# Kernel tuning notes

Measured on AMD Instinct MI355X. Metric: run time of the kernel, lower is better.

The kernel has to match this reference:

```python
import jax, jax.numpy as jnp
import numpy as np
import math

B, L, D, H, DFF, GEOM = 4, 768, 512, 8, 2048, 7
DK = D // H


def layer_norm(x, scale, bias, eps=1e-5):
    mu = jnp.mean(x, axis=-1, keepdims=True)
    var = jnp.mean(jnp.square(x - mu), axis=-1, keepdims=True)
    return (x - mu) * jax.lax.rsqrt(var + eps) * scale + bias


def setup_inputs() -> dict:
    key = jax.random.key(0)
    ks = jax.random.split(key, 20)
    s = 0.02
    inp = {
        "x": jax.random.normal(ks[0], (B, L, D), jnp.float32),
        "geom_feat": jax.random.uniform(ks[1], (B, L, L, GEOM), jnp.float32),
        "mask": jnp.ones((B, L), jnp.int32),
        # weights stored (in, out): y = x @ W + b, math-equivalent to torch Linear
        "Wq": jax.random.normal(ks[2], (D, D), jnp.float32) * s,
        "bq": jnp.zeros((D,), jnp.float32),
        "Wk": jax.random.normal(ks[3], (D, D), jnp.float32) * s,
        "bk": jnp.zeros((D,), jnp.float32),
        "Wv": jax.random.normal(ks[4], (D, D), jnp.float32) * s,
        "bv": jnp.zeros((D,), jnp.float32),
        "Wo": jax.random.normal(ks[5], (D, D), jnp.float32) * s,
        "bo": jnp.zeros((D,), jnp.float32),
        "Wg": jax.random.normal(ks[6], (GEOM, H), jnp.float32) * s,
        "bg": jnp.zeros((H,), jnp.float32),
        "Wgcn": jax.random.normal(ks[7], (D, D), jnp.float32) * s,
        "bgcn": jnp.zeros((D,), jnp.float32),
        "gcn_gate": jnp.float32(0.5),
        "W1": jax.random.normal(ks[8], (D, 2 * DFF), jnp.float32) * s,
        "b1": jnp.zeros((2 * DFF,), jnp.float32),
        "W2": jax.random.normal(ks[9], (DFF, D), jnp.float32) * s,
        "b2": jnp.zeros((D,), jnp.float32),
        "ln1_s": jnp.ones((D,), jnp.float32),
        "ln1_b": jnp.zeros((D,), jnp.float32),
        "ln2_s": jnp.ones((D,), jnp.float32),
        "ln2_b": jnp.zeros((D,), jnp.float32),
    }
    return inp


def reference(x, geom_feat, mask,
              Wq, bq, Wk, bk, Wv, bv, Wo, bo, Wg, bg,
              Wgcn, bgcn, gcn_gate, W1, b1, W2, b2,
              ln1_s, ln1_b, ln2_s, ln2_b):
    m = mask.astype(x.dtype)  # (B, L)
    # normalized adjacency from distance channel
    adj = jnp.exp(-geom_feat[..., 0] / 5.0)                 # (B, L, L)
    adj = adj * (m[:, :, None] * m[:, None, :])
    adj = adj / (jnp.sum(adj, axis=-1, keepdims=True) + 1e-6)

    h = layer_norm(x, ln1_s, ln1_b)                          # (B, L, D)

    # structure-guided attention
    Q = (h @ Wq + bq).reshape(B, L, H, DK)
    K = (h @ Wk + bk).reshape(B, L, H, DK)
    V = (h @ Wv + bv).reshape(B, L, H, DK)
    scores = jnp.einsum('blhd,bmhd->bhlm', Q, K) / math.sqrt(DK)
    bias = jnp.einsum('blmg,gh->bhlm', geom_feat, Wg) + bg[None, :, None, None]
    scores = scores + bias
    scores = jnp.where(mask[:, None, None, :] == 0, -10000.0, scores)
    attn = jax.nn.softmax(scores, axis=-1)
    ctx = jnp.einsum('bhlm,bmhd->blhd', attn, V).reshape(B, L, D)
    attn_out = ctx @ Wo + bo

    # dense GCN branch (exact GELU, matching torch nn.GELU default)
    g = h @ Wgcn + bgcn
    gcn_out = jax.nn.gelu(jnp.einsum('blm,bmd->bld', adj, g), approximate=False)

    x = x + attn_out + gcn_out * gcn_gate

    # gated feed-forward
    h2 = layer_norm(x, ln2_s, ln2_b)
    ff = h2 @ W1 + b1
    u, gate = ff[..., :DFF], ff[..., DFF:]
    x = x + (u * jax.nn.sigmoid(gate)) @ W2 + b2
    return x
```

## Files before the change

kernel.cpp:

```cpp
#include <hip/hip_runtime.h>
#include <hip/hip_bf16.h>
#include <math.h>

typedef __attribute__((ext_vector_type(8))) short bf8;
typedef __attribute__((ext_vector_type(4))) float f4;

typedef const __attribute__((address_space(1))) void* gas_t;
typedef __attribute__((address_space(3))) void* las_t;

__device__ __forceinline__ ushort f2bf(float x){
  union { float f; unsigned u; } v; v.f = x;
  unsigned r = (v.u + 0x7fffu + ((v.u >> 16) & 1u)) >> 16;
  return (ushort)r;
}
__device__ __forceinline__ float bf2f(ushort b){
  union { unsigned u; float f; } v; v.u = ((unsigned)b) << 16;
  return v.f;
}

struct GP {
  const ushort* A; long lda; long aBatch;
  const ushort* Bt; long ldb; long bBatch;
  const ushort* Bt2;
  int K;
  float* outf; ushort* outb;
  ushort* o1; ushort* o2; ushort* o3;
  const float* bias0; const float* bias1; const float* bias2; const float* bias3;
  const float* addf;
};

enum { EP_QKVG=0, EP_GCN, EP_ATTNOUT, EP_FF, EP_FINAL };

template<int EPI, bool DUAL>
__global__ __launch_bounds__(256)
void gemm_k(GP p) {
  __shared__ __align__(16) ushort As[64*64];
  __shared__ __align__(16) ushort Bs[64*64];
  __shared__ __align__(16) ushort Bs2[DUAL ? 64*64 : 8];
  const int tid = threadIdx.x;
  const int lane = tid & 63, w = tid >> 6;
  const int wm = w >> 1, wn = w & 1;
  const int g = lane >> 4, lr = lane & 15;
  const int lr8 = lane >> 3, sc = lane & 7;
  const int bm = blockIdx.x, bn = blockIdx.y, z = blockIdx.z;

  const ushort* Ab  = p.A  + (long)z*p.aBatch + (long)bm*64*p.lda;
  const ushort* Btb = p.Bt + (long)z*p.bBatch + (long)bn*64*p.ldb;
  const ushort* Bt2b = DUAL ? (p.Bt2 + (long)bn*64*p.ldb) : (const ushort*)nullptr;

  f4 acc[2][2] = {};
  f4 acc2[DUAL?2:1][DUAL?2:1] = {};

  for (int k0 = 0; k0 < p.K; k0 += 64) {
    #pragma unroll
    for (int i = 0; i < 2; ++i) {
      int row = i*32 + w*8 + lr8;
      const ushort* gsA = Ab + (long)row*p.lda + k0 + ((sc ^ (row & 7)) << 3);
      __builtin_amdgcn_global_load_lds((gas_t)gsA, (las_t)&As[(i*32 + w*8)*64], 16, 0, 0);
      const ushort* gsB = Btb + (long)row*p.ldb + k0 + ((sc ^ (row & 7)) << 3);
      __builtin_amdgcn_global_load_lds((gas_t)gsB, (las_t)&Bs[(i*32 + w*8)*64], 16, 0, 0);
      if (DUAL) {
        const ushort* gsB2 = Bt2b + (long)row*p.ldb + k0 + ((sc ^ (row & 7)) << 3);
        __builtin_amdgcn_global_load_lds((gas_t)gsB2, (las_t)&Bs2[(i*32 + w*8)*64], 16, 0, 0);
      }
    }
    __syncthreads();

    #pragma unroll
    for (int kw = 0; kw < 2; ++kw) {
      const int chunk = kw*4 + g;
      bf8 af[2], bfr[2], bf2[2];
      #pragma unroll
      for (int f = 0; f < 2; ++f) {
        int ar = wm*32 + f*16 + lr;
        af[f]  = *(const bf8*)&As[ar*64 + ((chunk ^ (ar & 7)) << 3)];
        int br = wn*32 + f*16 + lr;
        bfr[f] = *(const bf8*)&Bs[br*64 + ((chunk ^ (br & 7)) << 3)];
        if (DUAL) bf2[f] = *(const bf8*)&Bs2[br*64 + ((chunk ^ (br & 7)) << 3)];
      }
      #pragma unroll
      for (int fm = 0; fm < 2; ++fm)
        #pragma unroll
        for (int fn = 0; fn < 2; ++fn) {
          acc[fm][fn] = __builtin_amdgcn_mfma_f32_16x16x32_bf16(af[fm], bfr[fn], acc[fm][fn], 0,0,0);
          if (DUAL) acc2[fm][fn] = __builtin_amdgcn_mfma_f32_16x16x32_bf16(af[fm], bf2[fn], acc2[fm][fn], 0,0,0);
        }
    }
    __syncthreads();
  }

  #pragma unroll
  for (int fm = 0; fm < 2; ++fm)
  #pragma unroll
  for (int fn = 0; fn < 2; ++fn)
  #pragma unroll
  for (int i = 0; i < 4; ++i) {
    int grow = bm*64 + wm*32 + fm*16 + g*4 + i;
    int gcol = bn*64 + wn*32 + fn*16 + lr;
    float v = acc[fm][fn][i];
    if constexpr (EPI == EP_QKVG) {
      int sec = gcol >> 9, cc = gcol & 511;
      const float* bp = sec==0 ? p.bias0 : sec==1 ? p.bias1 : sec==2 ? p.bias2 : p.bias3;
      v += bp[cc];
      ushort bvv = f2bf(v);
      if (sec == 0)      p.outb[(long)grow*512 + cc] = bvv;
      else if (sec == 1) p.o1[(long)grow*512 + cc] = bvv;
      else {
        int b = grow / 768, l = grow - b*768;
        ushort* dst = (sec==2) ? p.o2 : p.o3;
        dst[((long)b*512 + cc)*768 + l] = bvv;
      }
    } else if constexpr (EPI == EP_GCN) {
      float ge = 0.5f * v * (1.f + erff(v * 0.70710678118f));
      p.outf[((long)z*768 + grow)*512 + gcol] = ge;
    } else if constexpr (EPI == EP_ATTNOUT) {
      p.outf[(long)grow*512 + gcol] = v + p.bias0[gcol];
    } else if constexpr (EPI == EP_FF) {
      float u = v + p.bias0[gcol];
      float gt = acc2[fm][fn][i] + p.bias0[2048 + gcol];
      float a = u / (1.f + expf(-gt));
      p.outb[(long)grow*2048 + gcol] = f2bf(a);
    } else if constexpr (EPI == EP_FINAL) {
      long idx = (long)grow*512 + gcol;
      p.outf[idx] = p.addf[idx] + v + p.bias0[gcol];
    }
  }
}

__global__ __launch_bounds__(256) void flash_k(const ushort* __restrict__ qg,
    const ushort* __restrict__ kg, const ushort* __restrict__ vtg,
    const ushort* __restrict__ biasg, ushort* __restrict__ ctx) {
  __shared__ __align__(16) ushort Ks[64*64];
  __shared__ __align__(16) ushort Vs[64*64];
  __shared__ __align__(16) ushort Ps[64*64];
  const int tid = threadIdx.x;
  const int lane = tid & 63, w = tid >> 6;
  const int g = lane >> 4, lr = lane & 15;
  const int qt = blockIdx.x, bh = blockIdx.y;
  const int b = bh >> 3, h = bh & 7;
  const int q0 = qt*64;

  bf8 aq[2];
  #pragma unroll
  for (int kk = 0; kk < 2; ++kk)
    aq[kk] = *(const bf8*)&qg[(long)(b*768 + q0 + w*16 + lr)*512 + h*64 + kk*32 + g*8];

  f4 o[4] = {};
  float mrow[4], lsum[4];
  #pragma unroll
  for (int i = 0; i < 4; ++i) { mrow[i] = -1e30f; lsum[i] = 0.f; }

  const int srow = tid >> 3, sc = tid & 7;

  for (int kt = 0; kt < 12; ++kt) {
    const int kbase = kt*64;
    #pragma unroll
    for (int ps = 0; ps < 2; ++ps) {
      int r = srow + ps*32;
      int sw = ((sc ^ (r & 7)) * 8);
      *(uint4*)&Ks[r*64 + sw] = *(const uint4*)&kg[(long)(b*768 + kbase + r)*512 + h*64 + sc*8];
      *(uint4*)&Vs[r*64 + sw] = *(const uint4*)&vtg[((long)b*512 + h*64 + r)*768 + kbase + sc*8];
    }
    __syncthreads();

    f4 s[4] = {};
    #pragma unroll
    for (int kn = 0; kn < 4; ++kn) {
      #pragma unroll
      for (int kk = 0; kk < 2; ++kk) {
        int row = kn*16 + lr;
        bf8 bk = *(const bf8*)&Ks[row*64 + (((kk*4+g) ^ (row & 7)) * 8)];
        s[kn] = __builtin_amdgcn_mfma_f32_16x16x32_bf16(aq[kk], bk, s[kn], 0,0,0);
      }
    }

    float pv[4][4];
    #pragma unroll
    for (int kn = 0; kn < 4; ++kn)
      #pragma unroll
      for (int i = 0; i < 4; ++i) {
        float bv = bf2f(biasg[((long)bh*768 + q0 + w*16 + g*4 + i)*768 + kbase + kn*16 + lr]);
        pv[kn][i] = s[kn][i]*0.125f + bv;
      }

    #pragma unroll
    for (int i = 0; i < 4; ++i) {
      float m2 = fmaxf(fmaxf(pv[0][i], pv[1][i]), fmaxf(pv[2][i], pv[3][i]));
      #pragma unroll
      for (int off = 1; off < 16; off <<= 1) m2 = fmaxf(m2, __shfl_xor(m2, off, 64));
      float mnew = fmaxf(mrow[i], m2);
      float scale = __expf(mrow[i] - mnew);
      mrow[i] = mnew;
      float psum = 0.f;
      #pragma unroll
      for (int kn = 0; kn < 4; ++kn) { pv[kn][i] = __expf(pv[kn][i] - mnew); psum += pv[kn][i]; }
      #pragma unroll
      for (int off = 1; off < 16; off <<= 1) psum += __shfl_xor(psum, off, 64);
      lsum[i] = lsum[i]*scale + psum;
      #pragma unroll
      for (int dn = 0; dn < 4; ++dn) o[dn][i] *= scale;
    }

    #pragma unroll
    for (int kn = 0; kn < 4; ++kn)
      #pragma unroll
      for (int i = 0; i < 4; ++i) {
        int row = w*16 + g*4 + i;
        int col = kn*16 + lr;
        Ps[row*64 + (((col >> 3) ^ (row & 7)) * 8) + (col & 7)] = f2bf(pv[kn][i]);
      }

    #pragma unroll
    for (int kk2 = 0; kk2 < 2; ++kk2) {
      int prow = w*16 + lr;
      bf8 pa = *(const bf8*)&Ps[prow*64 + (((kk2*4+g) ^ (prow & 7)) * 8)];
      #pragma unroll
      for (int dn = 0; dn < 4; ++dn) {
        int vrow = dn*16 + lr;
        bf8 bv = *(const bf8*)&Vs[vrow*64 + (((kk2*4+g) ^ (vrow & 7)) * 8)];
        o[dn] = __builtin_amdgcn_mfma_f32_16x16x32_bf16(pa, bv, o[dn], 0,0,0);
      }
    }
    __syncthreads();
  }

  #pragma unroll
  for (int i = 0; i < 4; ++i) {
    float inv = 1.f / lsum[i];
    #pragma unroll
    for (int dn = 0; dn < 4; ++dn)
      ctx[(long)(b*768 + q0 + w*16 + g*4 + i)*512 + h*64 + dn*16 + lr] = f2bf(o[dn][i]*inv);
  }
}

__global__ __launch_bounds__(256) void transpose_bf(const float* src, ushort* dst, int R, int C) {
  __shared__ float t[32][33];
  int r0 = blockIdx.x*32, c0 = blockIdx.y*32;
  int tr = threadIdx.x >> 5, tc = threadIdx.x & 31;
  #pragma unroll
  for (int i = 0; i < 4; ++i)
    t[tr + i*8][tc] = src[(long)(r0 + tr + i*8)*C + c0 + tc];
  __syncthreads();
  #pragma unroll
  for (int i = 0; i < 4; ++i)
    dst[(long)(c0 + tr + i*8)*R + r0 + tc] = f2bf(t[tc][tr + i*8]);
}

__global__ __launch_bounds__(256) void ln_k(const float* x, const float* gam, const float* bet, ushort* out) {
  int row = blockIdx.x, tid = threadIdx.x;
  long base = (long)row*512;
  float v0 = x[base+tid], v1 = x[base+tid+256];
  float s = v0+v1, q = v0*v0 + v1*v1;
  #pragma unroll
  for (int off=32; off>=1; off>>=1){ s += __shfl_down(s,off,64); q += __shfl_down(q,off,64); }
  __shared__ float red[8];
  int lane=tid&63, wave=tid>>6;
  if (lane==0){ red[wave]=s; red[4+wave]=q; }
  __syncthreads();
  if (tid==0){ red[0]=red[0]+red[1]+red[2]+red[3]; red[4]=red[4]+red[5]+red[6]+red[7]; }
  __syncthreads();
  float mu = red[0]*(1.f/512.f);
  float var = red[4]*(1.f/512.f) - mu*mu;
  float rs = rsqrtf(var + 1e-5f);
  out[base+tid]     = f2bf((v0-mu)*rs*gam[tid]     + bet[tid]);
  out[base+tid+256] = f2bf((v1-mu)*rs*gam[tid+256] + bet[tid+256]);
}

__global__ __launch_bounds__(256) void resid_ln2_k(const float* x, const float* ao, const float* gc,
    const float* gatep, const float* gam, const float* bet, float* xmid, ushort* h2) {
  int row = blockIdx.x, tid = threadIdx.x;
  long base = (long)row*512;
  float gate = *gatep;
  float v0 = x[base+tid]     + ao[base+tid]     + gc[base+tid]*gate;
  float v1 = x[base+tid+256] + ao[base+tid+256] + gc[base+tid+256]*gate;
  xmid[base+tid] = v0; xmid[base+tid+256] = v1;
  float s = v0+v1, q = v0*v0 + v1*v1;
  #pragma unroll
  for (int off=32; off>=1; off>>=1){ s += __shfl_down(s,off,64); q += __shfl_down(q,off,64); }
  __shared__ float red[8];
  int lane=tid&63, wave=tid>>6;
  if (lane==0){ red[wave]=s; red[4+wave]=q; }
  __syncthreads();
  if (tid==0){ red[0]=red[0]+red[1]+red[2]+red[3]; red[4]=red[4]+red[5]+red[6]+red[7]; }
  __syncthreads();
  float mu = red[0]*(1.f/512.f);
  float var = red[4]*(1.f/512.f) - mu*mu;
  float rs = rsqrtf(var + 1e-5f);
  h2[base+tid]     = f2bf((v0-mu)*rs*gam[tid]     + bet[tid]);
  h2[base+tid+256] = f2bf((v1-mu)*rs*gam[tid+256] + bet[tid+256]);
}

__global__ __launch_bounds__(256) void adjbias_k(const float* __restrict__ geom,
    const int* __restrict__ mask, const float* __restrict__ Wg, const float* __restrict__ bg,
    ushort* __restrict__ adjb, ushort* __restrict__ biasb) {
  int bl = blockIdx.x;
  int b = bl / 768, l = bl - b*768;
  int tid = threadIdx.x;
  __shared__ float wgs[56];
  __shared__ float bgs[8];
  if (tid < 56) wgs[tid] = Wg[tid];
  if (tid < 8)  bgs[tid] = bg[tid];
  __syncthreads();
  float ml = (float)mask[bl];
  float e[3]; float ssum = 0.f;
  #pragma unroll
  for (int j = 0; j < 3; ++j) {
    int m = tid + j*256;
    const float* gp = &geom[((long)bl*768 + m)*7];
    float g0 = gp[0], g1 = gp[1], g2 = gp[2], g3 = gp[3], g4 = gp[4], g5 = gp[5], g6 = gp[6];
    float mm = (float)mask[b*768 + m];
    e[j] = __expf(-g0*0.2f) * mm;
    ssum += e[j];
    #pragma unroll
    for (int hh = 0; hh < 8; ++hh) {
      float bv = bgs[hh] + g0*wgs[hh] + g1*wgs[8+hh] + g2*wgs[16+hh] + g3*wgs[24+hh]
               + g4*wgs[32+hh] + g5*wgs[40+hh] + g6*wgs[48+hh];
      biasb[((long)(b*8+hh)*768 + l)*768 + m] = f2bf(mm != 0.f ? bv : -10000.f);
    }
  }
  #pragma unroll
  for (int off=32; off>=1; off>>=1) ssum += __shfl_down(ssum, off, 64);
  __shared__ float red[4];
  int lane = tid & 63, wave = tid >> 6;
  if (lane == 0) red[wave] = ssum;
  __syncthreads();
  if (tid == 0) red[0] = red[0]+red[1]+red[2]+red[3];
  __syncthreads();
  float inv = ml / (ml*red[0] + 1e-6f);
  #pragma unroll
  for (int j = 0; j < 3; ++j)
    adjb[(long)bl*768 + tid + j*256] = f2bf(e[j] * inv);
}

extern "C" void kernel_launch(void* const* d_in, const int* in_sizes, int n_in,
                              void* d_out, int out_size, void* d_ws, size_t ws_size,
                              hipStream_t stream) {
  const float* x    = (const float*)d_in[0];
  const float* geom = (const float*)d_in[1];
  const int*   mask = (const int*)d_in[2];
  const float* Wq   = (const float*)d_in[3];
  const float* bq   = (const float*)d_in[4];
  const float* Wk   = (const float*)d_in[5];
  const float* bk   = (const float*)d_in[6];
  const float* Wv   = (const float*)d_in[7];
  const float* bv   = (const float*)d_in[8];
  const float* Wo   = (const float*)d_in[9];
  const float* bo   = (const float*)d_in[10];
  const float* Wg   = (const float*)d_in[11];
  const float* bg   = (const float*)d_in[12];
  const float* Wgcn = (const float*)d_in[13];
  const float* bgcn = (const float*)d_in[14];
  const float* gate = (const float*)d_in[15];
  const float* W1   = (const float*)d_in[16];
  const float* b1   = (const float*)d_in[17];
  const float* W2   = (const float*)d_in[18];
  const float* b2   = (const float*)d_in[19];
  const float* ln1s = (const float*)d_in[20];
  const float* ln1b = (const float*)d_in[21];
  const float* ln2s = (const float*)d_in[22];
  const float* ln2b = (const float*)d_in[23];
  float* out = (float*)d_out;

  char* wp = (char*)d_ws;
  auto alloc = [&](size_t bytes)->char* { char* r = wp; wp += (bytes + 255) & ~(size_t)255; return r; };
  ushort* wqkvgT = (ushort*)alloc(2048*512*2);
  ushort* woT    = (ushort*)alloc(512*512*2);
  ushort* w1T    = (ushort*)alloc(4096*512*2);
  ushort* w2T    = (ushort*)alloc(512*2048*2);
  ushort* hbf    = (ushort*)alloc(3072*512*2);
  ushort* qbf    = (ushort*)alloc(3072*512*2);
  ushort* kbf    = (ushort*)alloc(3072*512*2);
  ushort* vt     = (ushort*)alloc((size_t)4*512*768*2);
  ushort* gt     = (ushort*)alloc((size_t)4*512*768*2);
  ushort* adjb   = (ushort*)alloc((size_t)4*768*768*2);
  ushort* biasb  = (ushort*)alloc((size_t)32*768*768*2);
  ushort* ctx    = (ushort*)alloc(3072*512*2);
  float*  aout   = (float*)alloc(3072*512*4);
  float*  gcnr   = (float*)alloc(3072*512*4);
  float*  xmid   = (float*)alloc(3072*512*4);
  ushort* h2bf   = (ushort*)alloc(3072*512*2);
  ushort* act    = biasb;

  transpose_bf<<<dim3(16,16), 256, 0, stream>>>(Wq,   wqkvgT + 0*512*512, 512, 512);
  transpose_bf<<<dim3(16,16), 256, 0, stream>>>(Wk,   wqkvgT + 1*512*512, 512, 512);
  transpose_bf<<<dim3(16,16), 256, 0, stream>>>(Wv,   wqkvgT + 2*512*512, 512, 512);
  transpose_bf<<<dim3(16,16), 256, 0, stream>>>(Wgcn, wqkvgT + 3*512*512, 512, 512);
  transpose_bf<<<dim3(16,16), 256, 0, stream>>>(Wo,   woT, 512, 512);
  transpose_bf<<<dim3(16,128),256, 0, stream>>>(W1,   w1T, 512, 4096);
  transpose_bf<<<dim3(64,16), 256, 0, stream>>>(W2,   w2T, 2048, 512);

  ln_k<<<3072, 256, 0, stream>>>(x, ln1s, ln1b, hbf);
  adjbias_k<<<3072, 256, 0, stream>>>(geom, mask, Wg, bg, adjb, biasb);

  GP p{};
  p.A = hbf; p.lda = 512; p.aBatch = 0;
  p.Bt = wqkvgT; p.ldb = 512; p.bBatch = 0;
  p.K = 512;
  p.outb = qbf; p.o1 = kbf; p.o2 = vt; p.o3 = gt;
  p.bias0 = bq; p.bias1 = bk; p.bias2 = bv; p.bias3 = bgcn;
  gemm_k<EP_QKVG,false><<<dim3(48,32,1), 256, 0, stream>>>(p);

  flash_k<<<dim3(12,32), 256, 0, stream>>>(qbf, kbf, vt, biasb, ctx);

  p = GP{};
  p.A = adjb; p.lda = 768; p.aBatch = (long)768*768;
  p.Bt = gt; p.ldb = 768; p.bBatch = (long)512*768;
  p.K = 768;
  p.outf = gcnr;
  gemm_k<EP_GCN,false><<<dim3(12,8,4), 256, 0, stream>>>(p);

  p = GP{};
  p.A = ctx; p.lda = 512; p.aBatch = 0;
  p.Bt = woT; p.ldb = 512; p.bBatch = 0;
  p.K = 512;
  p.outf = aout; p.bias0 = bo;
  gemm_k<EP_ATTNOUT,false><<<dim3(48,8,1), 256, 0, stream>>>(p);

  resid_ln2_k<<<3072, 256, 0, stream>>>(x, aout, gcnr, gate, ln2s, ln2b, xmid, h2bf);

  p = GP{};
  p.A = h2bf; p.lda = 512; p.aBatch = 0;
  p.Bt = w1T; p.ldb = 512; p.bBatch = 0;
  p.Bt2 = w1T + (long)2048*512;
  p.K = 512;
  p.outb = act; p.bias0 = b1;
  gemm_k<EP_FF,true><<<dim3(48,32,1), 256, 0, stream>>>(p);

  p = GP{};
  p.A = act; p.lda = 2048; p.aBatch = 0;
  p.Bt = w2T; p.ldb = 2048; p.bBatch = 0;
  p.K = 2048;
  p.outf = out; p.bias0 = b2; p.addf = xmid;
  gemm_k<EP_FINAL,false><<<dim3(48,8,1), 256, 0, stream>>>(p);
}
```

Baseline: 309.0 us.

## Widen GEMM K-tile to 128, fold softmax scale into Q, batch weight transposes

The GEMM kernel now stages 128-wide K slices in LDS instead of 64, with a 16-way XOR swizzle. This halves the number of barrier pairs per output tile at the cost of more LDS per block. The 1/sqrt(dk) factor is applied to Q in the QKV epilogue rather than per score in the flash kernel. The seven separate weight-transpose launches are merged into one kernel that looks up each block's matrix from a table, cutting launch overhead. The larger LDS footprint may lower occupancy, and scaling Q before bf16 rounding changes rounding slightly.

```diff
diff --git a/kernel.cpp b/kernel.cpp
--- a/kernel.cpp
+++ b/kernel.cpp
@@ -34,14 +34,14 @@
 template<int EPI, bool DUAL>
 __global__ __launch_bounds__(256)
 void gemm_k(GP p) {
-  __shared__ __align__(16) ushort As[64*64];
-  __shared__ __align__(16) ushort Bs[64*64];
-  __shared__ __align__(16) ushort Bs2[DUAL ? 64*64 : 8];
+  __shared__ __align__(16) ushort As[64*128];
+  __shared__ __align__(16) ushort Bs[64*128];
+  __shared__ __align__(16) ushort Bs2[DUAL ? 64*128 : 8];
   const int tid = threadIdx.x;
   const int lane = tid & 63, w = tid >> 6;
   const int wm = w >> 1, wn = w & 1;
   const int g = lane >> 4, lr = lane & 15;
-  const int lr8 = lane >> 3, sc = lane & 7;
+  const int cg = lane & 15, rw = lane >> 4;
   const int bm = blockIdx.x, bn = blockIdx.y, z = blockIdx.z;
 
   const ushort* Ab  = p.A  + (long)z*p.aBatch + (long)bm*64*p.lda;
@@ -51,32 +51,32 @@
   f4 acc[2][2] = {};
   f4 acc2[DUAL?2:1][DUAL?2:1] = {};
 
-  for (int k0 = 0; k0 < p.K; k0 += 64) {
-    #pragma unroll
-    for (int i = 0; i < 2; ++i) {
-      int row = i*32 + w*8 + lr8;
-      const ushort* gsA = Ab + (long)row*p.lda + k0 + ((sc ^ (row & 7)) << 3);
-      __builtin_amdgcn_global_load_lds((gas_t)gsA, (las_t)&As[(i*32 + w*8)*64], 16, 0, 0);
-      const ushort* gsB = Btb + (long)row*p.ldb + k0 + ((sc ^ (row & 7)) << 3);
-      __builtin_amdgcn_global_load_lds((gas_t)gsB, (las_t)&Bs[(i*32 + w*8)*64], 16, 0, 0);
-      if (DUAL) {
-        const ushort* gsB2 = Bt2b + (long)row*p.ldb + k0 + ((sc ^ (row & 7)) << 3);
-        __builtin_amdgcn_global_load_lds((gas_t)gsB2, (las_t)&Bs2[(i*32 + w*8)*64], 16, 0, 0);
-      }
+  for (int k0 = 0; k0 < p.K; k0 += 128) {
+    #pragma unroll
+    for (int i = 0; i < 4; ++i) {
+      int row = i*16 + w*4 + rw;
+      int scol = (cg ^ (row & 15)) << 3;
+      __builtin_amdgcn_global_load_lds((gas_t)(Ab + (long)row*p.lda + k0 + scol),
+                                       (las_t)&As[(i*16 + w*4)*128], 16, 0, 0);
+      __builtin_amdgcn_global_load_lds((gas_t)(Btb + (long)row*p.ldb + k0 + scol),
+                                       (las_t)&Bs[(i*16 + w*4)*128], 16, 0, 0);
+      if (DUAL)
+        __builtin_amdgcn_global_load_lds((gas_t)(Bt2b + (long)row*p.ldb + k0 + scol),
+                                         (las_t)&Bs2[(i*16 + w*4)*128], 16, 0, 0);
     }
     __syncthreads();
 
     #pragma unroll
-    for (int kw = 0; kw < 2; ++kw) {
+    for (int kw = 0; kw < 4; ++kw) {
       const int chunk = kw*4 + g;
       bf8 af[2], bfr[2], bf2[2];
       #pragma unroll
       for (int f = 0; f < 2; ++f) {
         int ar = wm*32 + f*16 + lr;
-        af[f]  = *(const bf8*)&As[ar*64 + ((chunk ^ (ar & 7)) << 3)];
+        af[f]  = *(const bf8*)&As[ar*128 + ((chunk ^ (ar & 15)) << 3)];
         int br = wn*32 + f*16 + lr;
-        bfr[f] = *(const bf8*)&Bs[br*64 + ((chunk ^ (br & 7)) << 3)];
-        if (DUAL) bf2[f] = *(const bf8*)&Bs2[br*64 + ((chunk ^ (br & 7)) << 3)];
+        bfr[f] = *(const bf8*)&Bs[br*128 + ((chunk ^ (br & 15)) << 3)];
+        if (DUAL) bf2[f] = *(const bf8*)&Bs2[br*128 + ((chunk ^ (br & 15)) << 3)];
       }
       #pragma unroll
       for (int fm = 0; fm < 2; ++fm)
@@ -102,6 +102,7 @@
       int sec = gcol >> 9, cc = gcol & 511;
       const float* bp = sec==0 ? p.bias0 : sec==1 ? p.bias1 : sec==2 ? p.bias2 : p.bias3;
       v += bp[cc];
+      if (sec == 0) v *= 0.125f;
       ushort bvv = f2bf(v);
       if (sec == 0)      p.outb[(long)grow*512 + cc] = bvv;
       else if (sec == 1) p.o1[(long)grow*512 + cc] = bvv;
@@ -180,7 +181,7 @@
       #pragma unroll
       for (int i = 0; i < 4; ++i) {
         float bv = bf2f(biasg[((long)bh*768 + q0 + w*16 + g*4 + i)*768 + kbase + kn*16 + lr]);
-        pv[kn][i] = s[kn][i]*0.125f + bv;
+        pv[kn][i] = s[kn][i] + bv;
       }
 
     #pragma unroll
@@ -233,9 +234,22 @@
   }
 }
 
-__global__ __launch_bounds__(256) void transpose_bf(const float* src, ushort* dst, int R, int C) {
+struct TP {
+  const float* src[7]; ushort* dst[7];
+  int R[7], C[7]; int start[7]; int tilesX[7];
+};
+__global__ __launch_bounds__(256) void transpose_all(TP tp) {
   __shared__ float t[32][33];
-  int r0 = blockIdx.x*32, c0 = blockIdx.y*32;
+  int blk = blockIdx.x;
+  int m = 0;
+  #pragma unroll
+  for (int i = 1; i < 7; ++i) if (blk >= tp.start[i]) m = i;
+  int rel = blk - tp.start[m];
+  int bx = rel % tp.tilesX[m], by = rel / tp.tilesX[m];
+  const float* src = tp.src[m];
+  ushort* dst = tp.dst[m];
+  int R = tp.R[m], C = tp.C[m];
+  int r0 = bx*32, c0 = by*32;
   int tr = threadIdx.x >> 5, tc = threadIdx.x & 31;
   #pragma unroll
   for (int i = 0; i < 4; ++i)
@@ -381,13 +395,20 @@
   ushort* h2bf   = (ushort*)alloc(3072*512*2);
   ushort* act    = biasb;
 
-  transpose_bf<<<dim3(16,16), 256, 0, stream>>>(Wq,   wqkvgT + 0*512*512, 512, 512);
-  transpose_bf<<<dim3(16,16), 256, 0, stream>>>(Wk,   wqkvgT + 1*512*512, 512, 512);
-  transpose_bf<<<dim3(16,16), 256, 0, stream>>>(Wv,   wqkvgT + 2*512*512, 512, 512);
-  transpose_bf<<<dim3(16,16), 256, 0, stream>>>(Wgcn, wqkvgT + 3*512*512, 512, 512);
-  transpose_bf<<<dim3(16,16), 256, 0, stream>>>(Wo,   woT, 512, 512);
-  transpose_bf<<<dim3(16,128),256, 0, stream>>>(W1,   w1T, 512, 4096);
-  transpose_bf<<<dim3(64,16), 256, 0, stream>>>(W2,   w2T, 2048, 512);
+  TP tp;
+  const float* srcs[7] = { Wq, Wk, Wv, Wgcn, Wo, W1, W2 };
+  ushort* dsts[7] = { wqkvgT, wqkvgT + 512*512, wqkvgT + 2*512*512, wqkvgT + 3*512*512,
+                      woT, w1T, w2T };
+  int Rs[7] = { 512,512,512,512,512,512,2048 };
+  int Cs[7] = { 512,512,512,512,512,4096,512 };
+  int startAcc = 0;
+  for (int i = 0; i < 7; ++i) {
+    tp.src[i] = srcs[i]; tp.dst[i] = dsts[i]; tp.R[i] = Rs[i]; tp.C[i] = Cs[i];
+    tp.tilesX[i] = Rs[i] / 32;
+    tp.start[i] = startAcc;
+    startAcc += (Rs[i]/32) * (Cs[i]/32);
+  }
+  transpose_all<<<startAcc, 256, 0, stream>>>(tp);
 
   ln_k<<<3072, 256, 0, stream>>>(x, ln1s, ln1b, hbf);
   adjbias_k<<<3072, 256, 0, stream>>>(geom, mask, Wg, bg, adjb, biasb);
```

Result: faster. 290.3 us (-6.0%).
